# Kernel tuning notes

Hardware: AMD Instinct MI355X
Metric: run time of the kernel (lower is better)

The kernel has to match this reference:

```python
import jax, jax.numpy as jnp
import numpy as np

B, DIM, H, FFN = 16384, 1024, 16, 4096
HD = DIM // H
EPS = 1e-5


def _ln(x, g, b):
    mu = jnp.mean(x, axis=-1, keepdims=True)
    var = jnp.mean(jnp.square(x - mu), axis=-1, keepdims=True)
    return (x - mu) * jax.lax.rsqrt(var + EPS) * g + b


def setup_inputs() -> dict:
    key = jax.random.key(0)
    ks = jax.random.split(key, 20)
    s = 0.02
    d = {
        'm0': jax.random.normal(ks[0], (B, DIM), jnp.float32),
        'm1': jax.random.normal(ks[1], (B, DIM), jnp.float32),
        'm2': jax.random.normal(ks[2], (B, DIM), jnp.float32),
        'domain_rep': jax.random.normal(ks[3], (B, DIM), jnp.float32),
        'Wg': jax.random.normal(ks[4], (DIM, DIM), jnp.float32) * s,
        'bg': jnp.zeros((DIM,), jnp.float32),
        'Wq': jax.random.normal(ks[5], (DIM, DIM), jnp.float32) * s,
        'bq': jnp.zeros((DIM,), jnp.float32),
        'Wk': jax.random.normal(ks[6], (DIM, DIM), jnp.float32) * s,
        'bk': jnp.zeros((DIM,), jnp.float32),
        'Wv': jax.random.normal(ks[7], (DIM, DIM), jnp.float32) * s,
        'bv': jnp.zeros((DIM,), jnp.float32),
        'W1': jax.random.normal(ks[8], (DIM, FFN), jnp.float32) * s,
        'b1': jnp.zeros((FFN,), jnp.float32),
        'W2': jax.random.normal(ks[9], (FFN, DIM), jnp.float32) * s,
        'b2': jnp.zeros((DIM,), jnp.float32),
        'g1': jnp.ones((DIM,), jnp.float32),
        'beta1': jnp.zeros((DIM,), jnp.float32),
        'g2': jnp.ones((DIM,), jnp.float32),
        'beta2': jnp.zeros((DIM,), jnp.float32),
        'Ww': jax.random.normal(ks[10], (DIM, 3), jnp.float32) * s,
        'bw': jnp.zeros((3,), jnp.float32),
    }
    return d


def reference(m0, m1, m2, domain_rep, Wg, bg, Wq, bq, Wk, bk, Wv, bv,
              W1, b1, W2, b2, g1, beta1, g2, beta2, Ww, bw):
    mods = jnp.stack([m0, m1, m2], axis=1)            # [B, 3, DIM]
    global_rep = jnp.mean(mods, axis=1) @ Wg + bg      # [B, DIM]
    q = ((domain_rep + global_rep) @ Wq + bq).reshape(B, H, HD)
    k = (mods @ Wk + bk).reshape(B, 3, H, HD).transpose(0, 2, 1, 3)  # [B,H,3,HD]
    v = (mods @ Wv + bv).reshape(B, 3, H, HD).transpose(0, 2, 1, 3)
    scores = jnp.einsum('bhd,bhkd->bhk', q, k) / jnp.sqrt(jnp.float32(HD))
    attn = jax.nn.softmax(scores, axis=-1)             # [B,H,3]
    out = jnp.einsum('bhk,bhkd->bhd', attn, v).reshape(B, DIM)
    x = _ln(domain_rep + out, g1, beta1)
    ffn = jax.nn.relu(x @ W1 + b1) @ W2 + b2
    x = _ln(x + ffn, g2, beta2)
    return jax.nn.softmax(x @ Ww + bw, axis=-1)        # [B, 3]
```

## Files before the change

### kernel.cpp

```cpp
#include <hip/hip_runtime.h>

#define B_SZ 16384
#define DIM  1024
#define NH   16
#define HD   64
#define FFN_ 4096

typedef __bf16 bf16x8 __attribute__((ext_vector_type(8)));
typedef unsigned short u16x8 __attribute__((ext_vector_type(8)));
typedef float f32x4 __attribute__((ext_vector_type(4)));

__device__ __forceinline__ unsigned short f2bf(float x) {
    union { float f; unsigned int u; } v; v.f = x;
    unsigned int r = v.u + 0x7FFFu + ((v.u >> 16) & 1u);
    return (unsigned short)(r >> 16);
}
__device__ __forceinline__ float bf2f(unsigned short u) {
    union { unsigned int u32; float f; } v; v.u32 = ((unsigned int)u) << 16;
    return v.f;
}

__device__ __forceinline__ void gload16(const void* g, void* lds) {
    __builtin_amdgcn_global_load_lds(
        (__attribute__((address_space(1))) void*)g,
        (__attribute__((address_space(3))) void*)lds,
        16, 0, 0);
}

__global__ __launch_bounds__(256) void transpose_conv(
    const float* __restrict__ W, unsigned short* __restrict__ WT, int K, int N)
{
    __shared__ float tile[32][33];
    const int n0 = blockIdx.x * 32, k0 = blockIdx.y * 32;
    const int tx = threadIdx.x, ty = threadIdx.y;
    #pragma unroll
    for (int i = ty; i < 32; i += 8)
        tile[i][tx] = W[(size_t)(k0 + i) * N + n0 + tx];
    __syncthreads();
    #pragma unroll
    for (int i = ty; i < 32; i += 8)
        WT[(size_t)(n0 + i) * K + k0 + tx] = f2bf(tile[tx][i]);
}

__global__ __launch_bounds__(256) void concat_bias(
    const float* __restrict__ bk, const float* __restrict__ bv,
    float* __restrict__ bkv)
{
    int i = blockIdx.x * 256 + threadIdx.x;
    if (i < 1024) { bkv[i] = bk[i]; bkv[1024 + i] = bv[i]; }
}

__global__ __launch_bounds__(256) void conv_inputs(
    const float4* __restrict__ m0, const float4* __restrict__ m1,
    const float4* __restrict__ m2, ushort4* __restrict__ savg,
    ushort4* __restrict__ mjb, int n4)
{
    int idx = blockIdx.x * blockDim.x + threadIdx.x;
    int stride = gridDim.x * blockDim.x;
    const float k = 1.f / 3.f;
    for (int i = idx; i < n4; i += stride) {
        float4 a = m0[i], b = m1[i], c = m2[i];
        ushort4 us;
        us.x = f2bf((a.x + b.x + c.x) * k); us.y = f2bf((a.y + b.y + c.y) * k);
        us.z = f2bf((a.z + b.z + c.z) * k); us.w = f2bf((a.w + b.w + c.w) * k);
        savg[i] = us;
        if (mjb) {
            ushort4 ua, ub, uc;
            ua.x = f2bf(a.x); ua.y = f2bf(a.y); ua.z = f2bf(a.z); ua.w = f2bf(a.w);
            ub.x = f2bf(b.x); ub.y = f2bf(b.y); ub.z = f2bf(b.z); ub.w = f2bf(b.w);
            uc.x = f2bf(c.x); uc.y = f2bf(c.y); uc.z = f2bf(c.z); uc.w = f2bf(c.w);
            mjb[i] = ua; mjb[n4 + i] = ub; mjb[2 * n4 + i] = uc;
        }
    }
}

template <int MODE, bool AF32>
__global__ __launch_bounds__(256) void gemm2(
    const unsigned short* __restrict__ A,
    const float* __restrict__ A0, const float* __restrict__ A1,
    const float* __restrict__ A2, int chunk0, int Bc,
    const unsigned short* __restrict__ BT,
    const float* __restrict__ bias,
    const void* __restrict__ res,
    void* __restrict__ out, int K, int N)
{
    __shared__ __align__(16) char AsRaw[AF32 ? 32768 : 16384];
    __shared__ __align__(16) unsigned short Bs[2][4096];

    const int tid  = threadIdx.x;
    const int lane = tid & 63;
    const int wave = tid >> 6;
    const int wm = (wave >> 1) * 64;
    const int wn = (wave & 1) * 64;
    const int lr = lane & 15;
    const int quad = lane >> 4;

    const size_t rowB = (size_t)blockIdx.y * 128 + (tid >> 2);
    const int kcolB = (tid & 3) * 8;
    const unsigned short* Bg = BT + rowB * K + kcolB;

    const unsigned short* Ag = nullptr;
    const float* Agf = nullptr;
    if constexpr (AF32) {
        const int grow = blockIdx.x * 128;
        const int j = grow / Bc;
        const int b0 = (grow - j * Bc) + chunk0;
        const float* msrc = (j == 0) ? A0 : (j == 1) ? A1 : A2;
        const int arow = tid >> 3;
        const int jj = (tid & 7) ^ (arow & 7);
        Agf = msrc + (size_t)(b0 + arow) * DIM + jj * 4;
    } else {
        const size_t rowA = (size_t)blockIdx.x * 128 + (tid >> 2);
        Ag = A + rowA * K + kcolB;
    }

    f32x4 zero = {0.f, 0.f, 0.f, 0.f};
    f32x4 acc[4][4];
    #pragma unroll
    for (int i = 0; i < 4; ++i)
        #pragma unroll
        for (int j = 0; j < 4; ++j) acc[i][j] = zero;

    for (int k0 = 0; k0 < K; k0 += 64) {
        if constexpr (AF32) {
            float* Asf = (float*)AsRaw;
            #pragma unroll
            for (int h = 0; h < 2; ++h) {
                #pragma unroll
                for (int i = 0; i < 4; ++i)
                    gload16(Agf + (size_t)i * 32 * DIM + k0 + 32 * h,
                            (char*)(Asf + h * 4096) + i * 4096 + tid * 16);
            }
        } else {
            unsigned short* As = (unsigned short*)AsRaw;
            gload16(Ag + k0,                 (char*)As + tid * 16);
            gload16(Ag + (size_t)64 * K + k0,(char*)As + 4096 + tid * 16);
            gload16(Ag + k0 + 32,            (char*)As + 8192 + tid * 16);
            gload16(Ag + (size_t)64 * K + k0 + 32,
                                             (char*)As + 12288 + tid * 16);
        }
        gload16(Bg + k0,                  (char*)Bs[0] + tid * 16);
        gload16(Bg + (size_t)64 * K + k0, (char*)Bs[0] + 4096 + tid * 16);
        gload16(Bg + k0 + 32,             (char*)Bs[1] + tid * 16);
        gload16(Bg + (size_t)64 * K + k0 + 32,
                                          (char*)Bs[1] + 4096 + tid * 16);
        __syncthreads();

        #pragma unroll
        for (int h = 0; h < 2; ++h) {
            u16x8 af[4], bfr[4];
            if constexpr (AF32) {
                const float* Asf = (const float*)AsRaw + h * 4096;
                #pragma unroll
                for (int mi = 0; mi < 4; ++mi) {
                    const int r = wm + mi * 16 + lr;
                    const int s = lr & 7;
                    const float* rp = Asf + r * 32;
                    union { f32x4 f; unsigned int u[4]; } a0, a1;
                    a0.f = *(const f32x4*)(rp + (((quad << 1) ^ s) << 2));
                    a1.f = *(const f32x4*)(rp + ((((quad << 1) | 1) ^ s) << 2));
                    union { unsigned int i[4]; u16x8 v; } pk;
                    pk.i[0] = __builtin_amdgcn_perm(a0.u[1], a0.u[0], 0x07060302);
                    pk.i[1] = __builtin_amdgcn_perm(a0.u[3], a0.u[2], 0x07060302);
                    pk.i[2] = __builtin_amdgcn_perm(a1.u[1], a1.u[0], 0x07060302);
                    pk.i[3] = __builtin_amdgcn_perm(a1.u[3], a1.u[2], 0x07060302);
                    af[mi] = pk.v;
                }
            } else {
                const unsigned short* As =
                    (const unsigned short*)AsRaw + h * 4096;
                #pragma unroll
                for (int mi = 0; mi < 4; ++mi)
                    af[mi] = *(const u16x8*)&As[(wm + mi * 16 + lr) * 32 + quad * 8];
            }
            #pragma unroll
            for (int nj = 0; nj < 4; ++nj)
                bfr[nj] = *(const u16x8*)&Bs[h][(wn + nj * 16 + lr) * 32 + quad * 8];

            #pragma unroll
            for (int mi = 0; mi < 4; ++mi)
                #pragma unroll
                for (int nj = 0; nj < 4; ++nj)
                    acc[mi][nj] = __builtin_amdgcn_mfma_f32_16x16x32_bf16(
                        __builtin_bit_cast(bf16x8, af[mi]),
                        __builtin_bit_cast(bf16x8, bfr[nj]),
                        acc[mi][nj], 0, 0, 0);
        }
        __syncthreads();
    }

    const size_t rbase = (size_t)blockIdx.x * 128 + wm + quad * 4;
    const int cbase = blockIdx.y * 128 + wn + lr;
    #pragma unroll
    for (int mi = 0; mi < 4; ++mi) {
        #pragma unroll
        for (int nj = 0; nj < 4; ++nj) {
            const int gc = cbase + nj * 16;
            const float bv = bias[gc];
            #pragma unroll
            for (int r = 0; r < 4; ++r) {
                const size_t gr = rbase + mi * 16 + r;
                float v = acc[mi][nj][r] + bv;
                if (MODE == 1) v += ((const float*)res)[gr * N + gc];
                if (MODE == 2) v = v > 0.f ? v : 0.f;
                if (MODE == 4) {
                    v += bf2f(((const unsigned short*)res)[gr * N + gc]);
                    ((float*)out)[gr * N + gc] = v;
                } else {
                    ((unsigned short*)out)[gr * N + gc] = f2bf(v);
                }
            }
        }
    }
}

template <int MODE, bool CH>
__global__ __launch_bounds__(512, 2) void gemm256(
    const unsigned short* __restrict__ A, int chunk0, int Bc,
    const unsigned short* __restrict__ BT,
    const float* __restrict__ bias,
    const void* __restrict__ res,
    void* __restrict__ out, int K, int N)
{
    extern __shared__ __align__(16) char smem[];
    const int tid  = threadIdx.x;
    const int lane = tid & 63;
    const int wave = tid >> 6;
    const int wm = wave >> 2;
    const int wn = wave & 3;
    const int lr = lane & 15;
    const int quad = lane >> 4;

    const int srow  = tid >> 3;
    const int scolb = ((tid & 7) ^ (srow & 7)) << 4;

    size_t arow0;
    if constexpr (CH) {
        const int grow = blockIdx.x * 256;
        const int j = grow / Bc;
        arow0 = (size_t)j * B_SZ + chunk0 + (grow - j * Bc);
    } else {
        arow0 = (size_t)blockIdx.x * 256;
    }
    const unsigned short* Ag = A + (arow0 + srow) * (size_t)K + (scolb >> 1);
    const unsigned short* Bg =
        BT + ((size_t)blockIdx.y * 256 + srow) * (size_t)K + (scolb >> 1);
    char* lds0 = smem + tid * 16;

    const int cbx0 = (quad * 16) ^ ((lr & 7) << 4);
    const int cbx1 = (64 + quad * 16) ^ ((lr & 7) << 4);

    f32x4 zero = {0.f, 0.f, 0.f, 0.f};
    f32x4 acc[2][2][4][2];
    #pragma unroll
    for (int a = 0; a < 2; ++a)
        #pragma unroll
        for (int b = 0; b < 2; ++b)
            #pragma unroll
            for (int c = 0; c < 4; ++c)
                #pragma unroll
                for (int d = 0; d < 2; ++d) acc[a][b][c][d] = zero;

    u16x8 af[4][2], bf0[2][2], bf1[2][2];

#define STAGE_A(nb, m, t) do {                                          \
        const unsigned short* s_ = Ag + (size_t)((m) * 128) * K + (t) * 64; \
        char* d_ = lds0 + (nb) * 65536 + (m) * 16384;                   \
        gload16(s_, d_);                                                \
        gload16(s_ + (size_t)64 * K, d_ + 8192); } while (0)
#define STAGE_B(nb, n, t) do {                                          \
        const unsigned short* s_ = Bg + (size_t)((n) * 128) * K + (t) * 64; \
        char* d_ = lds0 + (nb) * 65536 + 32768 + (n) * 16384;           \
        gload16(s_, d_);                                                \
        gload16(s_ + (size_t)64 * K, d_ + 8192); } while (0)
#define LOADA(nb, hm) do {                                              \
        const char* b_ = smem + (nb) * 65536 + (hm) * 16384;            \
        _Pragma("unroll")                                               \
        for (int mi = 0; mi < 4; ++mi) {                                \
            const int ar_ = wm * 64 + mi * 16 + lr;                     \
            af[mi][0] = *(const u16x8*)(b_ + ar_ * 128 + cbx0);         \
            af[mi][1] = *(const u16x8*)(b_ + ar_ * 128 + cbx1); } } while (0)
#define LOADB(nb, hn, dst) do {                                         \
        const char* b_ = smem + (nb) * 65536 + 32768 + (hn) * 16384;    \
        _Pragma("unroll")                                               \
        for (int nj = 0; nj < 2; ++nj) {                                \
            const int br_ = wn * 32 + nj * 16 + lr;                     \
            dst[nj][0] = *(const u16x8*)(b_ + br_ * 128 + cbx0);        \
            dst[nj][1] = *(const u16x8*)(b_ + br_ * 128 + cbx1); } } while (0)
#define MFMAQ(QM, QN, BF)                                               \
        _Pragma("unroll")                                               \
        for (int mi = 0; mi < 4; ++mi)                                  \
        _Pragma("unroll")                                               \
        for (int nj = 0; nj < 2; ++nj)                                  \
        _Pragma("unroll")                                               \
        for (int ks = 0; ks < 2; ++ks)                                  \
            acc[QM][QN][mi][nj] = __builtin_amdgcn_mfma_f32_16x16x32_bf16( \
                __builtin_bit_cast(bf16x8, af[mi][ks]),                 \
                __builtin_bit_cast(bf16x8, BF[nj][ks]),                 \
                acc[QM][QN][mi][nj], 0, 0, 0);

    const int NT = K >> 6;
    STAGE_A(0, 0, 0); STAGE_B(0, 0, 0); STAGE_B(0, 1, 0); STAGE_A(0, 1, 0);
    asm volatile("s_waitcnt vmcnt(4)" ::: "memory");
    __builtin_amdgcn_s_barrier();

    for (int t = 0; t < NT; ++t) {
        const int nb = t & 1, ob = nb ^ 1;
        const bool more = (t + 1) < NT;
        LOADA(nb, 0); LOADB(nb, 0, bf0);
        if (more) { STAGE_A(ob, 0, t + 1);
                    asm volatile("s_waitcnt vmcnt(4)" ::: "memory"); }
        else      { asm volatile("s_waitcnt vmcnt(2)" ::: "memory"); }
        __builtin_amdgcn_s_barrier();
        __builtin_amdgcn_s_setprio(1);
        MFMAQ(0, 0, bf0);
        __builtin_amdgcn_s_setprio(0);
        __builtin_amdgcn_s_barrier();
        LOADB(nb, 1, bf1);
        if (more) { STAGE_B(ob, 0, t + 1);
                    asm volatile("s_waitcnt vmcnt(4)" ::: "memory"); }
        else      { asm volatile("s_waitcnt vmcnt(0)" ::: "memory"); }
        __builtin_amdgcn_s_barrier();
        __builtin_amdgcn_s_setprio(1);
        MFMAQ(0, 1, bf1);
        __builtin_amdgcn_s_setprio(0);
        __builtin_amdgcn_s_barrier();
        LOADA(nb, 1);
        if (more) { STAGE_B(ob, 1, t + 1);
                    asm volatile("s_waitcnt vmcnt(4)" ::: "memory"); }
        __builtin_amdgcn_s_barrier();
        __builtin_amdgcn_s_setprio(1);
        MFMAQ(1, 1, bf1);
        __builtin_amdgcn_s_setprio(0);
        __builtin_amdgcn_s_barrier();
        if (more) { STAGE_A(ob, 1, t + 1);
                    asm volatile("s_waitcnt vmcnt(4)" ::: "memory"); }
        __builtin_amdgcn_s_barrier();
        __builtin_amdgcn_s_setprio(1);
        MFMAQ(1, 0, bf0);
        __builtin_amdgcn_s_setprio(0);
        __builtin_amdgcn_s_barrier();
    }

#undef STAGE_A
#undef STAGE_B
#undef LOADA
#undef LOADB
#undef MFMAQ

    #pragma unroll
    for (int qm = 0; qm < 2; ++qm) {
        #pragma unroll
        for (int qn = 0; qn < 2; ++qn) {
            #pragma unroll
            for (int mi = 0; mi < 4; ++mi) {
                #pragma unroll
                for (int nj = 0; nj < 2; ++nj) {
                    const size_t gr0 = (size_t)blockIdx.x * 256 + qm * 128 +
                                       wm * 64 + mi * 16 + quad * 4;
                    const int gc = blockIdx.y * 256 + qn * 128 + wn * 32 +
                                   nj * 16 + lr;
                    const float bv = bias[gc];
                    f32x4 av = acc[qm][qn][mi][nj];
                    #pragma unroll
                    for (int r = 0; r < 4; ++r) {
                        const size_t gr = gr0 + r;
                        float v = av[r] + bv;
                        if (MODE == 1) v += ((const float*)res)[gr * N + gc];
                        if (MODE == 2) v = v > 0.f ? v : 0.f;
                        if (MODE == 4) {
                            v += bf2f(((const unsigned short*)res)[gr * N + gc]);
                            ((float*)out)[gr * N + gc] = v;
                        } else {
                            ((unsigned short*)out)[gr * N + gc] = f2bf(v);
                        }
                    }
                }
            }
        }
    }
}

__global__ __launch_bounds__(256) void attn_ln1(
    const unsigned short* __restrict__ qb,
    const unsigned short* __restrict__ KVb,
    const float* __restrict__ domain,
    const float* __restrict__ g1, const float* __restrict__ beta1,
    unsigned short* __restrict__ x1b, int chunk0, int Bc)
{
    const int b = blockIdx.x;
    const int t = threadIdx.x;
    const int d0 = t * 4;
    const size_t gbase = (size_t)(chunk0 + b) * DIM + d0;

    float q[4];
    { ushort4 u = *(const ushort4*)(qb + gbase);
      q[0] = bf2f(u.x); q[1] = bf2f(u.y); q[2] = bf2f(u.z); q[3] = bf2f(u.w); }

    float vv[3][4], s[3];
    #pragma unroll
    for (int j = 0; j < 3; ++j) {
        const size_t off = ((size_t)j * Bc + b) * 2048 + d0;
        ushort4 ku = *(const ushort4*)(KVb + off);
        ushort4 vu = *(const ushort4*)(KVb + off + 1024);
        float p = q[0] * bf2f(ku.x) + q[1] * bf2f(ku.y) +
                  q[2] * bf2f(ku.z) + q[3] * bf2f(ku.w);
        vv[j][0] = bf2f(vu.x); vv[j][1] = bf2f(vu.y);
        vv[j][2] = bf2f(vu.z); vv[j][3] = bf2f(vu.w);
        p += __shfl_down(p, 8, 16);
        p += __shfl_down(p, 4, 16);
        p += __shfl_down(p, 2, 16);
        p += __shfl_down(p, 1, 16);
        p = __shfl(p, 0, 16);
        s[j] = p * 0.125f;
    }
    float mx = fmaxf(s[0], fmaxf(s[1], s[2]));
    float e0 = __expf(s[0] - mx), e1 = __expf(s[1] - mx), e2 = __expf(s[2] - mx);
    float inv = 1.f / (e0 + e1 + e2);
    float a0 = e0 * inv, a1 = e1 * inv, a2 = e2 * inv;

    float4 dm = *(const float4*)(domain + gbase);
    float y[4];
    y[0] = dm.x + a0 * vv[0][0] + a1 * vv[1][0] + a2 * vv[2][0];
    y[1] = dm.y + a0 * vv[0][1] + a1 * vv[1][1] + a2 * vv[2][1];
    y[2] = dm.z + a0 * vv[0][2] + a1 * vv[1][2] + a2 * vv[2][2];
    y[3] = dm.w + a0 * vv[0][3] + a1 * vv[1][3] + a2 * vv[2][3];

    float sum = y[0] + y[1] + y[2] + y[3];
    float sq  = y[0]*y[0] + y[1]*y[1] + y[2]*y[2] + y[3]*y[3];
    #pragma unroll
    for (int off = 32; off > 0; off >>= 1) {
        sum += __shfl_down(sum, off, 64);
        sq  += __shfl_down(sq,  off, 64);
    }
    __shared__ float red[8];
    const int wv = t >> 6, ln = t & 63;
    if (ln == 0) { red[wv] = sum; red[4 + wv] = sq; }
    __syncthreads();
    float tot = red[0] + red[1] + red[2] + red[3];
    float tsq = red[4] + red[5] + red[6] + red[7];
    float mu = tot * (1.f / DIM);
    float var = tsq * (1.f / DIM) - mu * mu;
    float rs = rsqrtf(var + 1e-5f);
    #pragma unroll
    for (int i = 0; i < 4; ++i) {
        int d = d0 + i;
        float xv = (y[i] - mu) * rs * g1[d] + beta1[d];
        x1b[gbase + i] = f2bf(xv);
    }
}

__global__ __launch_bounds__(256) void ln2_proj(
    const float* __restrict__ xr,
    const float* __restrict__ g2, const float* __restrict__ beta2,
    const float* __restrict__ Ww, const float* __restrict__ bw,
    float* __restrict__ out, int chunk0)
{
    const int b = blockIdx.x;
    const int t = threadIdx.x;
    const int d0 = t * 4;
    const size_t base = (size_t)b * DIM + d0;
    float4 x = *(const float4*)(xr + base);
    float xs[4] = {x.x, x.y, x.z, x.w};

    float sum = xs[0] + xs[1] + xs[2] + xs[3];
    float sq  = xs[0]*xs[0] + xs[1]*xs[1] + xs[2]*xs[2] + xs[3]*xs[3];
    #pragma unroll
    for (int off = 32; off > 0; off >>= 1) {
        sum += __shfl_down(sum, off, 64);
        sq  += __shfl_down(sq,  off, 64);
    }
    __shared__ float red[8];
    const int wv = t >> 6, ln = t & 63;
    if (ln == 0) { red[wv] = sum; red[4 + wv] = sq; }
    __syncthreads();
    float tot = red[0] + red[1] + red[2] + red[3];
    float tsq = red[4] + red[5] + red[6] + red[7];
    float mu = tot * (1.f / DIM);
    float var = tsq * (1.f / DIM) - mu * mu;
    float rs = rsqrtf(var + 1e-5f);

    float p0 = 0.f, p1 = 0.f, p2 = 0.f;
    #pragma unroll
    for (int i = 0; i < 4; ++i) {
        int d = d0 + i;
        float xv = (xs[i] - mu) * rs * g2[d] + beta2[d];
        p0 += xv * Ww[d * 3 + 0];
        p1 += xv * Ww[d * 3 + 1];
        p2 += xv * Ww[d * 3 + 2];
    }
    #pragma unroll
    for (int off = 32; off > 0; off >>= 1) {
        p0 += __shfl_down(p0, off, 64);
        p1 += __shfl_down(p1, off, 64);
        p2 += __shfl_down(p2, off, 64);
    }
    __shared__ float pr[12];
    if (ln == 0) { pr[wv] = p0; pr[4 + wv] = p1; pr[8 + wv] = p2; }
    __syncthreads();
    if (t == 0) {
        float l0 = pr[0] + pr[1] + pr[2] + pr[3] + bw[0];
        float l1 = pr[4] + pr[5] + pr[6] + pr[7] + bw[1];
        float l2 = pr[8] + pr[9] + pr[10] + pr[11] + bw[2];
        float m = fmaxf(l0, fmaxf(l1, l2));
        float e0 = __expf(l0 - m), e1 = __expf(l1 - m), e2 = __expf(l2 - m);
        float inv = 1.f / (e0 + e1 + e2);
        out[(size_t)(chunk0 + b) * 3 + 0] = e0 * inv;
        out[(size_t)(chunk0 + b) * 3 + 1] = e1 * inv;
        out[(size_t)(chunk0 + b) * 3 + 2] = e2 * inv;
    }
}

extern "C" void kernel_launch(void* const* d_in, const int* in_sizes, int n_in,
                              void* d_out, int out_size, void* d_ws, size_t ws_size,
                              hipStream_t stream)
{
    const float* m0     = (const float*)d_in[0];
    const float* m1     = (const float*)d_in[1];
    const float* m2     = (const float*)d_in[2];
    const float* domain = (const float*)d_in[3];
    const float* Wg = (const float*)d_in[4];  const float* bg = (const float*)d_in[5];
    const float* Wq = (const float*)d_in[6];  const float* bq = (const float*)d_in[7];
    const float* Wk = (const float*)d_in[8];  const float* bk = (const float*)d_in[9];
    const float* Wv = (const float*)d_in[10]; const float* bv = (const float*)d_in[11];
    const float* W1 = (const float*)d_in[12]; const float* b1 = (const float*)d_in[13];
    const float* W2 = (const float*)d_in[14]; const float* b2 = (const float*)d_in[15];
    const float* g1 = (const float*)d_in[16]; const float* beta1 = (const float*)d_in[17];
    const float* g2 = (const float*)d_in[18]; const float* beta2 = (const float*)d_in[19];
    const float* Ww = (const float*)d_in[20]; const float* bw = (const float*)d_in[21];
    float* out = (float*)d_out;

    char* ws = (char*)d_ws;
    const size_t MiB = 1ull << 20;

    static int attr_ok = -1;
    if (attr_ok < 0) {
        hipError_t e = hipFuncSetAttribute(
            reinterpret_cast<const void*>(&gemm256<0, false>),
            hipFuncAttributeMaxDynamicSharedMemorySize, 131072);
        if (e == hipSuccess) e = hipFuncSetAttribute(
            reinterpret_cast<const void*>(&gemm256<0, true>),
            hipFuncAttributeMaxDynamicSharedMemorySize, 131072);
        if (e == hipSuccess) e = hipFuncSetAttribute(
            reinterpret_cast<const void*>(&gemm256<1, false>),
            hipFuncAttributeMaxDynamicSharedMemorySize, 131072);
        if (e == hipSuccess) e = hipFuncSetAttribute(
            reinterpret_cast<const void*>(&gemm256<2, false>),
            hipFuncAttributeMaxDynamicSharedMemorySize, 131072);
        if (e == hipSuccess) e = hipFuncSetAttribute(
            reinterpret_cast<const void*>(&gemm256<4, false>),
            hipFuncAttributeMaxDynamicSharedMemorySize, 131072);
        attr_ok = (e == hipSuccess) ? 1 : 0;
    }

    unsigned short* wgT  = (unsigned short*)(ws);
    unsigned short* wqT  = (unsigned short*)(ws + 2 * MiB);
    unsigned short* wkvT = (unsigned short*)(ws + 4 * MiB);
    unsigned short* w1T  = (unsigned short*)(ws + 8 * MiB);
    unsigned short* w2T  = (unsigned short*)(ws + 16 * MiB);
    float*          bkv  = (float*)(ws + 24 * MiB);

    const dim3 tb(32, 8);
    transpose_conv<<<dim3(DIM / 32, DIM / 32), tb, 0, stream>>>(Wg, wgT, DIM, DIM);
    transpose_conv<<<dim3(DIM / 32, DIM / 32), tb, 0, stream>>>(Wq, wqT, DIM, DIM);
    transpose_conv<<<dim3(DIM / 32, DIM / 32), tb, 0, stream>>>(Wk, wkvT, DIM, DIM);
    transpose_conv<<<dim3(DIM / 32, DIM / 32), tb, 0, stream>>>(
        Wv, wkvT + (size_t)DIM * DIM, DIM, DIM);
    transpose_conv<<<dim3(FFN_ / 32, DIM / 32), tb, 0, stream>>>(W1, w1T, DIM, FFN_);
    transpose_conv<<<dim3(DIM / 32, FFN_ / 32), tb, 0, stream>>>(W2, w2T, FFN_, DIM);
    concat_bias<<<4, 256, 0, stream>>>(bk, bv, bkv);

    char* base = ws + 25 * MiB;
    const int n4 = B_SZ * DIM / 4;

    if (attr_ok) {
        const bool FULLT = ws_size >= 282 * MiB;
        const bool MIDT  = !FULLT && ws_size >= 250 * MiB;
        if (FULLT || MIDT) {
            const int BcKV = FULLT ? 8192 : 4096;
            unsigned short* mjb  = (unsigned short*)(base);
            unsigned short* qb   = (unsigned short*)(base + 96 * MiB);
            unsigned short* x1b  = (unsigned short*)(base + 128 * MiB);
            char* shared         = base + 160 * MiB;
            unsigned short* savg = (unsigned short*)(shared);
            unsigned short* dq   = (unsigned short*)(shared + 32 * MiB);
            unsigned short* KVb  = (unsigned short*)(shared);
            unsigned short* h1   = (unsigned short*)(base);
            float*          xr   = (float*)(shared);

            conv_inputs<<<8192, 256, 0, stream>>>(
                (const float4*)m0, (const float4*)m1, (const float4*)m2,
                (ushort4*)savg, (ushort4*)mjb, n4);

            gemm256<1, false><<<dim3(B_SZ / 256, DIM / 256), 512, 131072, stream>>>(
                savg, 0, 0, wgT, bg, domain, dq, DIM, DIM);
            gemm256<0, false><<<dim3(B_SZ / 256, DIM / 256), 512, 131072, stream>>>(
                dq, 0, 0, wqT, bq, nullptr, qb, DIM, DIM);

            for (int c = 0; c < B_SZ / BcKV; ++c) {
                const int chunk0 = c * BcKV;
                gemm256<0, true><<<dim3(3 * BcKV / 256, 2048 / 256), 512, 131072, stream>>>(
                    mjb, chunk0, BcKV, wkvT, bkv, nullptr, KVb, DIM, 2048);
                attn_ln1<<<BcKV, 256, 0, stream>>>(qb, KVb, domain, g1, beta1,
                                                   x1b, chunk0, BcKV);
            }

            gemm256<2, false><<<dim3(B_SZ / 256, FFN_ / 256), 512, 131072, stream>>>(
                x1b, 0, 0, w1T, b1, nullptr, h1, DIM, FFN_);
            gemm256<4, false><<<dim3(B_SZ / 256, DIM / 256), 512, 131072, stream>>>(
                h1, 0, 0, w2T, b2, x1b, xr, FFN_, DIM);
            ln2_proj<<<B_SZ, 256, 0, stream>>>(xr, g2, beta2, Ww, bw, out, 0);
            return;
        }
        const bool T2 = ws_size >= 185 * MiB;
        const int BcKV = T2 ? 8192 : 4096;
        const int BcF  = T2 ? 8192 : 4096;
        unsigned short* savg = (unsigned short*)(base);
        unsigned short* qb   = (unsigned short*)(base);
        unsigned short* x1b  = (unsigned short*)(base + 32 * MiB);
        unsigned short* dq   = (unsigned short*)(base + 64 * MiB);
        unsigned short* KVb  = (unsigned short*)(base + 64 * MiB);
        unsigned short* h1   = (unsigned short*)(base + 64 * MiB);
        float*          xr   = (float*)(base + 64 * MiB + (size_t)BcF * FFN_ * 2);

        conv_inputs<<<8192, 256, 0, stream>>>(
            (const float4*)m0, (const float4*)m1, (const float4*)m2,
            (ushort4*)savg, nullptr, n4);

        gemm256<1, false><<<dim3(B_SZ / 256, DIM / 256), 512, 131072, stream>>>(
            savg, 0, 0, wgT, bg, domain, dq, DIM, DIM);
        gemm256<0, false><<<dim3(B_SZ / 256, DIM / 256), 512, 131072, stream>>>(
            dq, 0, 0, wqT, bq, nullptr, qb, DIM, DIM);

        for (int c = 0; c < B_SZ / BcKV; ++c) {
            const int chunk0 = c * BcKV;
            gemm2<0, true><<<dim3(3 * BcKV / 128, 2048 / 128), 256, 0, stream>>>(
                nullptr, m0, m1, m2, chunk0, BcKV, wkvT, bkv, nullptr, KVb,
                DIM, 2048);
            attn_ln1<<<BcKV, 256, 0, stream>>>(qb, KVb, domain, g1, beta1,
                                               x1b, chunk0, BcKV);
        }
        for (int c = 0; c < B_SZ / BcF; ++c) {
            const int chunk0 = c * BcF;
            const unsigned short* x1c = x1b + (size_t)chunk0 * DIM;
            gemm256<2, false><<<dim3(BcF / 256, FFN_ / 256), 512, 131072, stream>>>(
                x1c, 0, 0, w1T, b1, nullptr, h1, DIM, FFN_);
            gemm256<4, false><<<dim3(BcF / 256, DIM / 256), 512, 131072, stream>>>(
                h1, 0, 0, w2T, b2, x1c, xr, FFN_, DIM);
            ln2_proj<<<BcF, 256, 0, stream>>>(xr, g2, beta2, Ww, bw, out, chunk0);
        }
        return;
    }

    {
        const bool T2 = ws_size >= 185 * MiB;
        const int BcKV = T2 ? 8192 : 4096;
        const int BcF  = T2 ? 8192 : 4096;
        unsigned short* savg = (unsigned short*)(base);
        unsigned short* qb   = (unsigned short*)(base);
        unsigned short* x1b  = (unsigned short*)(base + 32 * MiB);
        unsigned short* dq   = (unsigned short*)(base + 64 * MiB);
        unsigned short* KVb  = (unsigned short*)(base + 64 * MiB);
        unsigned short* h1   = (unsigned short*)(base + 64 * MiB);
        float*          xr   = (float*)(base + 64 * MiB + (size_t)BcF * FFN_ * 2);

        conv_inputs<<<8192, 256, 0, stream>>>(
            (const float4*)m0, (const float4*)m1, (const float4*)m2,
            (ushort4*)savg, nullptr, n4);

        gemm2<1, false><<<dim3(B_SZ / 128, DIM / 128), 256, 0, stream>>>(
            savg, nullptr, nullptr, nullptr, 0, 0, wgT, bg, domain, dq, DIM, DIM);
        gemm2<0, false><<<dim3(B_SZ / 128, DIM / 128), 256, 0, stream>>>(
            dq, nullptr, nullptr, nullptr, 0, 0, wqT, bq, nullptr, qb, DIM, DIM);

        for (int c = 0; c < B_SZ / BcKV; ++c) {
            const int chunk0 = c * BcKV;
            gemm2<0, true><<<dim3(3 * BcKV / 128, 2048 / 128), 256, 0, stream>>>(
                nullptr, m0, m1, m2, chunk0, BcKV, wkvT, bkv, nullptr, KVb,
                DIM, 2048);
            attn_ln1<<<BcKV, 256, 0, stream>>>(qb, KVb, domain, g1, beta1,
                                               x1b, chunk0, BcKV);
        }
        for (int c = 0; c < B_SZ / BcF; ++c) {
            const int chunk0 = c * BcF;
            const unsigned short* x1c = x1b + (size_t)chunk0 * DIM;
            gemm2<2, false><<<dim3(BcF / 128, FFN_ / 128), 256, 0, stream>>>(
                x1c, nullptr, nullptr, nullptr, 0, 0, w1T, b1, nullptr, h1,
                DIM, FFN_);
            gemm2<4, false><<<dim3(BcF / 128, DIM / 128), 256, 0, stream>>>(
                h1, nullptr, nullptr, nullptr, 0, 0, w2T, b2, x1c, xr,
                FFN_, DIM);
            ln2_proj<<<BcF, 256, 0, stream>>>(xr, g2, beta2, Ww, bw, out, chunk0);
        }
    }
}
```

Measured before the change: 960.3 us.

## Fold Wg into Wq and fuse global and query projections into one K-concat GEMM

Precomputes the bf16 product Wg·Wq (split-K partial GEMM plus reduction) and a fused bias bg·Wq+bq. The query projection then becomes a single GEMM over the concatenated [domain, mean-modality] inputs with K=2048. This removes the intermediate dq tensor and one GEMM launch, at the cost of extra per-call weight preprocessing, a bf16 copy of domain_rep, and an extra rounding step on the fused weight.

Result: slower. 1.013 ms (+5.5%).

```diff
diff --git a/kernel.cpp b/kernel.cpp
--- a/kernel.cpp
+++ b/kernel.cpp
@@ -42,6 +42,18 @@
         WT[(size_t)(n0 + i) * K + k0 + tx] = f2bf(tile[tx][i]);
 }
 
+__global__ __launch_bounds__(256) void conv_w(
+    const float4* __restrict__ W, ushort4* __restrict__ O, int n4)
+{
+    int i = blockIdx.x * 256 + threadIdx.x;
+    if (i < n4) {
+        float4 v = W[i];
+        ushort4 u;
+        u.x = f2bf(v.x); u.y = f2bf(v.y); u.z = f2bf(v.z); u.w = f2bf(v.w);
+        O[i] = u;
+    }
+}
+
 __global__ __launch_bounds__(256) void concat_bias(
     const float* __restrict__ bk, const float* __restrict__ bv,
     float* __restrict__ bkv)
@@ -50,10 +62,109 @@
     if (i < 1024) { bkv[i] = bk[i]; bkv[1024 + i] = bv[i]; }
 }
 
+__global__ __launch_bounds__(256) void bgq_kernel(
+    const unsigned short* __restrict__ wqT, const float* __restrict__ bg,
+    const float* __restrict__ bq, float* __restrict__ bgq)
+{
+    int n = blockIdx.x * 256 + threadIdx.x;
+    if (n < 1024) {
+        const unsigned short* wr = wqT + (size_t)n * 1024;
+        float s = bq[n];
+        for (int j = 0; j < 1024; ++j) s += bg[j] * bf2f(wr[j]);
+        bgq[n] = s;
+    }
+}
+
+__global__ __launch_bounds__(256) void wgq_partial(
+    const unsigned short* __restrict__ A,
+    const unsigned short* __restrict__ BT,
+    float* __restrict__ R)
+{
+    __shared__ __align__(16) unsigned short As[8192];
+    __shared__ __align__(16) unsigned short Bs[8192];
+    const int tid = threadIdx.x, lane = tid & 63, wave = tid >> 6;
+    const int wm = (wave >> 1) * 64, wn = (wave & 1) * 64;
+    const int lr = lane & 15, quad = lane >> 4;
+    const int koff = blockIdx.z * 128;
+    const size_t rowA = blockIdx.x * 128 + (tid >> 2);
+    const size_t rowB = blockIdx.y * 128 + (tid >> 2);
+    const int kcol = (tid & 3) * 8;
+    const unsigned short* Ag = A + rowA * 1024 + kcol + koff;
+    const unsigned short* Bg = BT + rowB * 1024 + kcol + koff;
+
+    f32x4 zero = {0.f, 0.f, 0.f, 0.f};
+    f32x4 acc[4][4];
+    #pragma unroll
+    for (int i = 0; i < 4; ++i)
+        #pragma unroll
+        for (int j = 0; j < 4; ++j) acc[i][j] = zero;
+
+    for (int k0 = 0; k0 < 128; k0 += 64) {
+        gload16(Ag + k0,                   (char*)As + tid * 16);
+        gload16(Ag + (size_t)64 * 1024 + k0, (char*)As + 4096 + tid * 16);
+        gload16(Ag + k0 + 32,              (char*)As + 8192 + tid * 16);
+        gload16(Ag + (size_t)64 * 1024 + k0 + 32,
+                                           (char*)As + 12288 + tid * 16);
+        gload16(Bg + k0,                   (char*)Bs + tid * 16);
+        gload16(Bg + (size_t)64 * 1024 + k0, (char*)Bs + 4096 + tid * 16);
+        gload16(Bg + k0 + 32,              (char*)Bs + 8192 + tid * 16);
+        gload16(Bg + (size_t)64 * 1024 + k0 + 32,
+                                           (char*)Bs + 12288 + tid * 16);
+        __syncthreads();
+        #pragma unroll
+        for (int h = 0; h < 2; ++h) {
+            u16x8 af[4], bfr[4];
+            #pragma unroll
+            for (int mi = 0; mi < 4; ++mi)
+                af[mi] = *(const u16x8*)&As[h * 4096 + (wm + mi * 16 + lr) * 32 + quad * 8];
+            #pragma unroll
+            for (int nj = 0; nj < 4; ++nj)
+                bfr[nj] = *(const u16x8*)&Bs[h * 4096 + (wn + nj * 16 + lr) * 32 + quad * 8];
+            #pragma unroll
+            for (int mi = 0; mi < 4; ++mi)
+                #pragma unroll
+                for (int nj = 0; nj < 4; ++nj)
+                    acc[mi][nj] = __builtin_amdgcn_mfma_f32_16x16x32_bf16(
+                        __builtin_bit_cast(bf16x8, af[mi]),
+                        __builtin_bit_cast(bf16x8, bfr[nj]),
+                        acc[mi][nj], 0, 0, 0);
+        }
+        __syncthreads();
+    }
+    float* Rz = R + (size_t)blockIdx.z * 1024 * 1024;
+    const size_t rbase = (size_t)blockIdx.x * 128 + wm + quad * 4;
+    const int cbase = blockIdx.y * 128 + wn + lr;
+    #pragma unroll
+    for (int mi = 0; mi < 4; ++mi)
+        #pragma unroll
+        for (int nj = 0; nj < 4; ++nj)
+            #pragma unroll
+            for (int r = 0; r < 4; ++r)
+                Rz[(rbase + mi * 16 + r) * 1024 + cbase + nj * 16] = acc[mi][nj][r];
+}
+
+__global__ __launch_bounds__(256) void reduce_wgq(
+    const float4* __restrict__ R, ushort4* __restrict__ O)
+{
+    int i = blockIdx.x * 256 + threadIdx.x;
+    if (i < 262144) {
+        float4 s = R[i];
+        #pragma unroll
+        for (int kc = 1; kc < 8; ++kc) {
+            float4 v = R[(size_t)kc * 262144 + i];
+            s.x += v.x; s.y += v.y; s.z += v.z; s.w += v.w;
+        }
+        ushort4 u;
+        u.x = f2bf(s.x); u.y = f2bf(s.y); u.z = f2bf(s.z); u.w = f2bf(s.w);
+        O[i] = u;
+    }
+}
+
 __global__ __launch_bounds__(256) void conv_inputs(
     const float4* __restrict__ m0, const float4* __restrict__ m1,
-    const float4* __restrict__ m2, ushort4* __restrict__ savg,
-    ushort4* __restrict__ mjb, int n4)
+    const float4* __restrict__ m2, const float4* __restrict__ dm,
+    ushort4* __restrict__ savg, ushort4* __restrict__ mjb,
+    ushort4* __restrict__ domb, int n4)
 {
     int idx = blockIdx.x * blockDim.x + threadIdx.x;
     int stride = gridDim.x * blockDim.x;
@@ -70,6 +181,12 @@
             ub.x = f2bf(b.x); ub.y = f2bf(b.y); ub.z = f2bf(b.z); ub.w = f2bf(b.w);
             uc.x = f2bf(c.x); uc.y = f2bf(c.y); uc.z = f2bf(c.z); uc.w = f2bf(c.w);
             mjb[i] = ua; mjb[n4 + i] = ub; mjb[2 * n4 + i] = uc;
+        }
+        if (domb) {
+            float4 d = dm[i];
+            ushort4 ud;
+            ud.x = f2bf(d.x); ud.y = f2bf(d.y); ud.z = f2bf(d.z); ud.w = f2bf(d.w);
+            domb[i] = ud;
         }
     }
 }
@@ -216,11 +333,14 @@
 
 template <int MODE, bool CH>
 __global__ __launch_bounds__(512, 2) void gemm256(
-    const unsigned short* __restrict__ A, int chunk0, int Bc,
+    const unsigned short* __restrict__ A,
+    const unsigned short* __restrict__ A2p,
+    int chunk0, int Bc,
     const unsigned short* __restrict__ BT,
+    const unsigned short* __restrict__ BT2p,
     const float* __restrict__ bias,
     const void* __restrict__ res,
-    void* __restrict__ out, int K, int N)
+    void* __restrict__ out, int K, int KK, int N)
 {
     extern __shared__ __align__(16) char smem[];
     const int tid  = threadIdx.x;
@@ -243,8 +363,13 @@
         arow0 = (size_t)blockIdx.x * 256;
     }
     const unsigned short* Ag = A + (arow0 + srow) * (size_t)K + (scolb >> 1);
+    const unsigned short* Ag2 =
+        (A2p ? A2p : A) + (arow0 + srow) * (size_t)K + (scolb >> 1);
     const unsigned short* Bg =
         BT + ((size_t)blockIdx.y * 256 + srow) * (size_t)K + (scolb >> 1);
+    const unsigned short* Bg2 =
+        (BT2p ? BT2p : BT) + ((size_t)blockIdx.y * 256 + srow) * (size_t)K +
+        (scolb >> 1);
     char* lds0 = smem + tid * 16;
 
     const int cbx0 = (quad * 16) ^ ((lr & 7) << 4);
@@ -263,13 +388,20 @@
 
     u16x8 af[4][2], bf0[2][2], bf1[2][2];
 
-#define STAGE_A(nb, m, t) do {                                          \
-        const unsigned short* s_ = Ag + (size_t)((m) * 128) * K + (t) * 64; \
+    const int NT = KK >> 6;
+    const int hNT = K >> 6;
+
+#define STAGE_A(nb, m, t) do { const int tt_ = (t);                     \
+        const unsigned short* s_ = ((tt_ < hNT)                         \
+            ? Ag  + (size_t)tt_ * 64                                    \
+            : Ag2 + (size_t)(tt_ - hNT) * 64) + (size_t)((m) * 128) * K;\
         char* d_ = lds0 + (nb) * 65536 + (m) * 16384;                   \
         gload16(s_, d_);                                                \
         gload16(s_ + (size_t)64 * K, d_ + 8192); } while (0)
-#define STAGE_B(nb, n, t) do {                                          \
-        const unsigned short* s_ = Bg + (size_t)((n) * 128) * K + (t) * 64; \
+#define STAGE_B(nb, n, t) do { const int tt_ = (t);                     \
+        const unsigned short* s_ = ((tt_ < hNT)                         \
+            ? Bg  + (size_t)tt_ * 64                                    \
+            : Bg2 + (size_t)(tt_ - hNT) * 64) + (size_t)((n) * 128) * K;\
         char* d_ = lds0 + (nb) * 65536 + 32768 + (n) * 16384;           \
         gload16(s_, d_);                                                \
         gload16(s_ + (size_t)64 * K, d_ + 8192); } while (0)
@@ -299,7 +431,6 @@
                 __builtin_bit_cast(bf16x8, BF[nj][ks]),                 \
                 acc[QM][QN][mi][nj], 0, 0, 0);
 
-    const int NT = K >> 6;
     STAGE_A(0, 0, 0); STAGE_B(0, 0, 0); STAGE_B(0, 1, 0); STAGE_A(0, 1, 0);
     asm volatile("s_waitcnt vmcnt(4)" ::: "memory");
     __builtin_amdgcn_s_barrier();
@@ -553,15 +684,17 @@
         attr_ok = (e == hipSuccess) ? 1 : 0;
     }
 
-    unsigned short* wgT  = (unsigned short*)(ws);
-    unsigned short* wqT  = (unsigned short*)(ws + 2 * MiB);
-    unsigned short* wkvT = (unsigned short*)(ws + 4 * MiB);
-    unsigned short* w1T  = (unsigned short*)(ws + 8 * MiB);
-    unsigned short* w2T  = (unsigned short*)(ws + 16 * MiB);
+    unsigned short* wqT  = (unsigned short*)(ws);
+    unsigned short* wkvT = (unsigned short*)(ws + 2 * MiB);
+    unsigned short* w1T  = (unsigned short*)(ws + 6 * MiB);
+    unsigned short* w2T  = (unsigned short*)(ws + 14 * MiB);
+    unsigned short* slot22 = (unsigned short*)(ws + 22 * MiB);
     float*          bkv  = (float*)(ws + 24 * MiB);
+    float*          bgq  = (float*)(ws + 24 * MiB + 16384);
+    char* base = ws + 25 * MiB;
+    const int n4 = B_SZ * DIM / 4;
 
     const dim3 tb(32, 8);
-    transpose_conv<<<dim3(DIM / 32, DIM / 32), tb, 0, stream>>>(Wg, wgT, DIM, DIM);
     transpose_conv<<<dim3(DIM / 32, DIM / 32), tb, 0, stream>>>(Wq, wqT, DIM, DIM);
     transpose_conv<<<dim3(DIM / 32, DIM / 32), tb, 0, stream>>>(Wk, wkvT, DIM, DIM);
     transpose_conv<<<dim3(DIM / 32, DIM / 32), tb, 0, stream>>>(
@@ -570,48 +703,56 @@
     transpose_conv<<<dim3(DIM / 32, FFN_ / 32), tb, 0, stream>>>(W2, w2T, FFN_, DIM);
     concat_bias<<<4, 256, 0, stream>>>(bk, bv, bkv);
 
-    char* base = ws + 25 * MiB;
-    const int n4 = B_SZ * DIM / 4;
+    if (attr_ok && ws_size >= 250 * MiB) {
+        const bool FULLT = ws_size >= 282 * MiB;
+        const int BcKV = FULLT ? 8192 : 4096;
+        unsigned short* mjb  = (unsigned short*)(base);
+        unsigned short* qb   = (unsigned short*)(base + 96 * MiB);
+        unsigned short* x1b  = (unsigned short*)(base + 128 * MiB);
+        float*          R8   = (float*)(base + 128 * MiB);
+        unsigned short* savg = (unsigned short*)(base + 160 * MiB);
+        unsigned short* wgB  = (unsigned short*)(base + 160 * MiB);
+        unsigned short* domb = (unsigned short*)(base + 192 * MiB);
+        unsigned short* KVb  = (unsigned short*)(base + 160 * MiB);
+        unsigned short* h1   = (unsigned short*)(base);
+        float*          xr   = (float*)(base + 160 * MiB);
+        unsigned short* wgqT = slot22;
+
+        conv_w<<<1024, 256, 0, stream>>>((const float4*)Wg, (ushort4*)wgB,
+                                         DIM * DIM / 4);
+        bgq_kernel<<<4, 256, 0, stream>>>(wqT, bg, bq, bgq);
+        wgq_partial<<<dim3(8, 8, 8), 256, 0, stream>>>(wqT, wgB, R8);
+        reduce_wgq<<<1024, 256, 0, stream>>>((const float4*)R8, (ushort4*)wgqT);
+
+        conv_inputs<<<8192, 256, 0, stream>>>(
+            (const float4*)m0, (const float4*)m1, (const float4*)m2,
+            (const float4*)domain, (ushort4*)savg, (ushort4*)mjb,
+            (ushort4*)domb, n4);
+
+        gemm256<0, false><<<dim3(B_SZ / 256, DIM / 256), 512, 131072, stream>>>(
+            domb, savg, 0, 0, wqT, wgqT, bgq, nullptr, qb, DIM, 2 * DIM, DIM);
+
+        for (int c = 0; c < B_SZ / BcKV; ++c) {
+            const int chunk0 = c * BcKV;
+            gemm256<0, true><<<dim3(3 * BcKV / 256, 2048 / 256), 512, 131072, stream>>>(
+                mjb, nullptr, chunk0, BcKV, wkvT, nullptr, bkv, nullptr, KVb,
+                DIM, DIM, 2048);
+            attn_ln1<<<BcKV, 256, 0, stream>>>(qb, KVb, domain, g1, beta1,
+                                               x1b, chunk0, BcKV);
+        }
+
+        gemm256<2, false><<<dim3(B_SZ / 256, FFN_ / 256), 512, 131072, stream>>>(
+            x1b, nullptr, 0, 0, w1T, nullptr, b1, nullptr, h1, DIM, DIM, FFN_);
+        gemm256<4, false><<<dim3(B_SZ / 256, DIM / 256), 512, 131072, stream>>>(
+            h1, nullptr, 0, 0, w2T, nullptr, b2, x1b, xr, FFN_, FFN_, DIM);
+        ln2_proj<<<B_SZ, 256, 0, stream>>>(xr, g2, beta2, Ww, bw, out, 0);
+        return;
+    }
+
+    unsigned short* wgT = slot22;
+    transpose_conv<<<dim3(DIM / 32, DIM / 32), tb, 0, stream>>>(Wg, wgT, DIM, DIM);
 
     if (attr_ok) {
-        const bool FULLT = ws_size >= 282 * MiB;
-        const bool MIDT  = !FULLT && ws_size >= 250 * MiB;
-        if (FULLT || MIDT) {
-            const int BcKV = FULLT ? 8192 : 4096;
-            unsigned short* mjb  = (unsigned short*)(base);
-            unsigned short* qb   = (unsigned short*)(base + 96 * MiB);
-            unsigned short* x1b  = (unsigned short*)(base + 128 * MiB);
-            char* shared         = base + 160 * MiB;
-            unsigned short* savg = (unsigned short*)(shared);
-            unsigned short* dq   = (unsigned short*)(shared + 32 * MiB);
-            unsigned short* KVb  = (unsigned short*)(shared);
-            unsigned short* h1   = (unsigned short*)(base);
-            float*          xr   = (float*)(shared);
-
-            conv_inputs<<<8192, 256, 0, stream>>>(
-                (const float4*)m0, (const float4*)m1, (const float4*)m2,
-                (ushort4*)savg, (ushort4*)mjb, n4);
-
-            gemm256<1, false><<<dim3(B_SZ / 256, DIM / 256), 512, 131072, stream>>>(
-                savg, 0, 0, wgT, bg, domain, dq, DIM, DIM);
-            gemm256<0, false><<<dim3(B_SZ / 256, DIM / 256), 512, 131072, stream>>>(
-                dq, 0, 0, wqT, bq, nullptr, qb, DIM, DIM);
-
-            for (int c = 0; c < B_SZ / BcKV; ++c) {
-                const int chunk0 = c * BcKV;
-                gemm256<0, true><<<dim3(3 * BcKV / 256, 2048 / 256), 512, 131072, stream>>>(
-                    mjb, chunk0, BcKV, wkvT, bkv, nullptr, KVb, DIM, 2048);
-                attn_ln1<<<BcKV, 256, 0, stream>>>(qb, KVb, domain, g1, beta1,
-                                                   x1b, chunk0, BcKV);
-            }
-
-            gemm256<2, false><<<dim3(B_SZ / 256, FFN_ / 256), 512, 131072, stream>>>(
-                x1b, 0, 0, w1T, b1, nullptr, h1, DIM, FFN_);
-            gemm256<4, false><<<dim3(B_SZ / 256, DIM / 256), 512, 131072, stream>>>(
-                h1, 0, 0, w2T, b2, x1b, xr, FFN_, DIM);
-            ln2_proj<<<B_SZ, 256, 0, stream>>>(xr, g2, beta2, Ww, bw, out, 0);
-            return;
-        }
         const bool T2 = ws_size >= 185 * MiB;
         const int BcKV = T2 ? 8192 : 4096;
         const int BcF  = T2 ? 8192 : 4096;
@@ -625,12 +766,12 @@
 
         conv_inputs<<<8192, 256, 0, stream>>>(
             (const float4*)m0, (const float4*)m1, (const float4*)m2,
-            (ushort4*)savg, nullptr, n4);
+            nullptr, (ushort4*)savg, nullptr, nullptr, n4);
 
         gemm256<1, false><<<dim3(B_SZ / 256, DIM / 256), 512, 131072, stream>>>(
-            savg, 0, 0, wgT, bg, domain, dq, DIM, DIM);
+            savg, nullptr, 0, 0, wgT, nullptr, bg, domain, dq, DIM, DIM, DIM);
         gemm256<0, false><<<dim3(B_SZ / 256, DIM / 256), 512, 131072, stream>>>(
-            dq, 0, 0, wqT, bq, nullptr, qb, DIM, DIM);
+            dq, nullptr, 0, 0, wqT, nullptr, bq, nullptr, qb, DIM, DIM, DIM);
 
         for (int c = 0; c < B_SZ / BcKV; ++c) {
             const int chunk0 = c * BcKV;
@@ -644,9 +785,9 @@
             const int chunk0 = c * BcF;
             const unsigned short* x1c = x1b + (size_t)chunk0 * DIM;
             gemm256<2, false><<<dim3(BcF / 256, FFN_ / 256), 512, 131072, stream>>>(
-                x1c, 0, 0, w1T, b1, nullptr, h1, DIM, FFN_);
+                x1c, nullptr, 0, 0, w1T, nullptr, b1, nullptr, h1, DIM, DIM, FFN_);
             gemm256<4, false><<<dim3(BcF / 256, DIM / 256), 512, 131072, stream>>>(
-                h1, 0, 0, w2T, b2, x1c, xr, FFN_, DIM);
+                h1, nullptr, 0, 0, w2T, nullptr, b2, x1c, xr, FFN_, FFN_, DIM);
             ln2_proj<<<BcF, 256, 0, stream>>>(xr, g2, beta2, Ww, bw, out, chunk0);
         }
         return;
@@ -666,7 +807,7 @@
 
         conv_inputs<<<8192, 256, 0, stream>>>(
             (const float4*)m0, (const float4*)m1, (const float4*)m2,
-            (ushort4*)savg, nullptr, n4);
+            nullptr, (ushort4*)savg, nullptr, nullptr, n4);
 
         gemm2<1, false><<<dim3(B_SZ / 128, DIM / 128), 256, 0, stream>>>(
             savg, nullptr, nullptr, nullptr, 0, 0, wgT, bg, domain, dq, DIM, DIM);
```
